# Kernel optimization log

Hardware: AMD Instinct MI355X
Metric: run time of the kernel (lower is better)

The kernel has to match this reference:

```python
import math
import jax, jax.numpy as jnp
import numpy as np


def _procrustes_R(H):
    # H: [B, 3, 3]. Rotation R = V @ U^T with reflection fix (det(R) >= 0),
    # matching torch.svd convention (v = V, not V^T).
    u, s, vh = jnp.linalg.svd(H)
    v = jnp.swapaxes(vh, -1, -2)                       # [B,3,3]
    r = jnp.einsum('bij,bkj->bik', v, u)               # V @ U^T
    det = jnp.linalg.det(r)                            # [B]
    sign = jnp.where(det < 0, -1.0, 1.0)               # flip last column of V (reflect = diag(1,1,-1))
    flip = jnp.stack([jnp.ones_like(sign), jnp.ones_like(sign), sign], axis=-1)[:, None, :]
    v = v * flip
    return jnp.einsum('bij,bkj->bik', v, u)


def setup_inputs() -> dict:
    key = jax.random.key(0)
    k1, k2, k3, k4 = jax.random.split(key, 4)
    B, D, N, M = 8, 512, 2048, 2048
    return {
        'src_embedding': jax.random.normal(k1, (B, D, N), dtype=jnp.float32),
        'tgt_embedding': jax.random.normal(k2, (B, D, M), dtype=jnp.float32),
        'src': jax.random.normal(k3, (B, 3, N), dtype=jnp.float32),
        'tgt': jax.random.normal(k4, (B, 3, M), dtype=jnp.float32),
    }


def reference(src_embedding, tgt_embedding, src, tgt):
    d_k = src_embedding.shape[1]
    # attention correspondence: scores[b,n,m]
    scores = jnp.einsum('bdn,bdm->bnm', src_embedding, tgt_embedding) / math.sqrt(d_k)
    scores = jax.nn.softmax(scores, axis=2)
    # soft correspondence of src points in tgt: [B,3,N]
    src_corr = jnp.einsum('bdm,bnm->bdn', tgt, scores)
    src_mean = src.mean(axis=2, keepdims=True)          # [B,3,1]
    src_centered = src - src_mean
    src_corr_centered = src_corr - src_corr.mean(axis=2, keepdims=True)
    H = jnp.einsum('bin,bjn->bij', src_centered, src_corr_centered)  # [B,3,3]
    R = _procrustes_R(H)
    t = jnp.einsum('bij,bjk->bik', -R, src_mean) + tgt.mean(axis=2, keepdims=True)
    return R, t.reshape(src.shape[0], 3)
```

## Files before the change

kernel.cpp:

```cpp
#include <hip/hip_runtime.h>
#include <hip/hip_bf16.h>

#define BQ 8
#define DIM 512
#define NN 2048
#define MM 2048
#define MSPLIT 16

typedef __attribute__((ext_vector_type(8))) short short8;
typedef __attribute__((ext_vector_type(8))) unsigned short ushort8;
typedef __attribute__((ext_vector_type(4))) float floatx4;

#define GLOAD_LDS(gp, lp) \
    __builtin_amdgcn_global_load_lds( \
        (const __attribute__((address_space(1))) void*)(gp), \
        (__attribute__((address_space(3))) void*)(lp), 16, 0, 0)


static __device__ __forceinline__ unsigned short f2bf(float x) {
    __hip_bfloat16 h = __float2bfloat16(x);
    return *(unsigned short*)&h;
}

__global__ __launch_bounds__(256) void transpose_cast_kernel(
    const float* __restrict__ src_emb,
    const float* __restrict__ tgt_emb,
    __hip_bfloat16* __restrict__ Abf,
    __hip_bfloat16* __restrict__ Bbf)
{
    const int n0 = blockIdx.x * 64;
    const int d0 = blockIdx.y * 64;
    const int b  = blockIdx.z & 7;
    const int which = blockIdx.z >> 3;

    const float* in = (which == 0 ? src_emb : tgt_emb) + (size_t)b * DIM * NN;
    __hip_bfloat16* out = (which == 0 ? Abf : Bbf) + (size_t)b * NN * DIM;

    __shared__ float tl[64][65];

    const int t = threadIdx.x;

    {
        const int u = t & 15;
        const int r = t >> 4;
        #pragma unroll
        for (int rr = r; rr < 64; rr += 16) {
            float4 v = *(const float4*)&in[(size_t)(d0 + rr) * NN + n0 + u * 4];
            tl[rr][u * 4 + 0] = v.x;
            tl[rr][u * 4 + 1] = v.y;
            tl[rr][u * 4 + 2] = v.z;
            tl[rr][u * 4 + 3] = v.w;
        }
    }
    __syncthreads();

    {
        const int u = t & 7;
        const int r = t >> 3;
        #pragma unroll
        for (int rn = r; rn < 64; rn += 32) {
            ushort8 o;
            #pragma unroll
            for (int j = 0; j < 8; j++)
                o[j] = f2bf(tl[u * 8 + j][rn]);
            *(ushort8*)&out[(size_t)(n0 + rn) * DIM + d0 + u * 8] = o;
        }
    }
}

__global__ __launch_bounds__(256, 2) void attn_mfma_kernel(
    const __hip_bfloat16* __restrict__ Abf,
    const __hip_bfloat16* __restrict__ Bbf,
    const float* __restrict__ tgt,
    float* __restrict__ part)
{
    const int nt = blockIdx.x;
    const int qt = blockIdx.y;
    const int b  = blockIdx.z;
    const int t  = threadIdx.x;
    const int wave = t >> 6;
    const int lane = t & 63;
    const int lm   = lane & 15;
    const int quad = lane >> 4;
    const int wn   = wave * 32;

    __shared__ short As[128 * 64];
    __shared__ short Bs[128 * 64];

    const __hip_bfloat16* Abase = Abf + ((size_t)(b * NN + nt * 128)) * DIM;
    const int m0 = qt * 128;
    const __hip_bfloat16* Bbase = Bbf + ((size_t)(b * MM + m0)) * DIM;
    const float* Tb = tgt + (size_t)b * 3 * MM;

    const float SCALE = 0.044194173824159216f * 1.4426950408889634f;

    const int r8 = lane >> 3;
    const int c8 = lane & 7;
    const int cc = c8 ^ r8;
    const __hip_bfloat16* gA = Abase + (size_t)(wn + r8) * DIM + cc * 8;
    const __hip_bfloat16* gB = Bbase + (size_t)(wn + r8) * DIM + cc * 8;
    short* lA = &As[wn * 64];
    short* lB = &Bs[wn * 64];

    floatx4 acc[2][8];
    #pragma unroll
    for (int i = 0; i < 2; i++)
        #pragma unroll
        for (int j = 0; j < 8; j++)
            acc[i][j] = (floatx4){0.f, 0.f, 0.f, 0.f};

    #pragma unroll
    for (int kt = 0; kt < 8; kt++) {
        #pragma unroll
        for (int i = 0; i < 4; i++) {
            GLOAD_LDS(gA + kt * 64 + (size_t)i * 8 * DIM, lA + i * 512);
            GLOAD_LDS(gB + kt * 64 + (size_t)i * 8 * DIM, lB + i * 512);
        }
        __syncthreads();

        #pragma unroll
        for (int ks = 0; ks < 2; ks++) {
            const int pc = (((ks * 4 + quad) ^ (lane & 7)) * 8);
            short8 af0 = *(const short8*)&As[(wn +      lm) * 64 + pc];
            short8 af1 = *(const short8*)&As[(wn + 16 + lm) * 64 + pc];
            #pragma unroll
            for (int j = 0; j < 8; j++) {
                short8 bf = *(const short8*)&Bs[(j * 16 + lm) * 64 + pc];
                acc[0][j] = __builtin_amdgcn_mfma_f32_16x16x32_bf16(af0, bf, acc[0][j], 0, 0, 0);
                acc[1][j] = __builtin_amdgcn_mfma_f32_16x16x32_bf16(af1, bf, acc[1][j], 0, 0, 0);
            }
        }
        __syncthreads();
    }

    float v0[8], v1[8], v2[8];
    #pragma unroll
    for (int j = 0; j < 8; j++) {
        int vc = m0 + j * 16 + lm;
        v0[j] = Tb[vc];
        v1[j] = Tb[MM + vc];
        v2[j] = Tb[2 * MM + vc];
    }

    const size_t slot = (size_t)(b * MSPLIT + qt) * NN;
    #pragma unroll
    for (int i = 0; i < 2; i++) {
        float l4[4] = {0,0,0,0};
        float o0[4] = {0,0,0,0};
        float o1[4] = {0,0,0,0};
        float o2[4] = {0,0,0,0};
        #pragma unroll
        for (int j = 0; j < 8; j++) {
            #pragma unroll
            for (int r = 0; r < 4; r++) {
                float e = __builtin_amdgcn_exp2f(acc[i][j][r] * SCALE);
                l4[r] += e;
                o0[r] += e * v0[j];
                o1[r] += e * v1[j];
                o2[r] += e * v2[j];
            }
        }
        #pragma unroll
        for (int m = 1; m <= 8; m <<= 1) {
            #pragma unroll
            for (int r = 0; r < 4; r++) {
                l4[r] += __shfl_xor(l4[r], m);
                o0[r] += __shfl_xor(o0[r], m);
                o1[r] += __shfl_xor(o1[r], m);
                o2[r] += __shfl_xor(o2[r], m);
            }
        }
        if (lm == 0) {
            #pragma unroll
            for (int r = 0; r < 4; r++) {
                int n = nt * 128 + wn + i * 16 + quad * 4 + r;
                ((float4*)part)[slot + n] = make_float4(l4[r], o0[r], o1[r], o2[r]);
            }
        }
    }
}

__global__ __launch_bounds__(256) void head_kernel(
    const float* __restrict__ ws,
    const float* __restrict__ src,
    const float* __restrict__ tgt,
    float* __restrict__ out)
{
    const int b = blockIdx.x;
    const int t = threadIdx.x;

    float pp[3][3] = {};
    float sc[3] = {0,0,0};
    float ss[3] = {0,0,0};
    float st[3] = {0,0,0};

    const float4* w4 = (const float4*)ws;
    const float* S = src + (size_t)b * 3 * NN;
    const float* T = tgt + (size_t)b * 3 * MM;

    for (int n = t; n < NN; n += 256) {
        float l = 0.f, y0 = 0.f, y1 = 0.f, y2 = 0.f;
        #pragma unroll
        for (int q = 0; q < 16; q++) {
            float4 p = w4[(size_t)(b * 16 + q) * NN + n];
            l += p.x; y0 += p.y; y1 += p.z; y2 += p.w;
        }
        float inv = 1.0f / l;
        float c0 = y0 * inv;
        float c1 = y1 * inv;
        float c2 = y2 * inv;
        float s0 = S[n], s1 = S[NN + n], s2 = S[2 * NN + n];
        sc[0] += c0; sc[1] += c1; sc[2] += c2;
        ss[0] += s0; ss[1] += s1; ss[2] += s2;
        st[0] += T[n]; st[1] += T[MM + n]; st[2] += T[2 * MM + n];
        pp[0][0] += s0 * c0; pp[0][1] += s0 * c1; pp[0][2] += s0 * c2;
        pp[1][0] += s1 * c0; pp[1][1] += s1 * c1; pp[1][2] += s1 * c2;
        pp[2][0] += s2 * c0; pp[2][1] += s2 * c1; pp[2][2] += s2 * c2;
    }

    float vals[18];
    vals[0] = ss[0]; vals[1] = ss[1]; vals[2] = ss[2];
    vals[3] = sc[0]; vals[4] = sc[1]; vals[5] = sc[2];
    vals[6] = st[0]; vals[7] = st[1]; vals[8] = st[2];
    vals[9]  = pp[0][0]; vals[10] = pp[0][1]; vals[11] = pp[0][2];
    vals[12] = pp[1][0]; vals[13] = pp[1][1]; vals[14] = pp[1][2];
    vals[15] = pp[2][0]; vals[16] = pp[2][1]; vals[17] = pp[2][2];

    #pragma unroll
    for (int m = 1; m <= 32; m <<= 1)
        #pragma unroll
        for (int c = 0; c < 18; c++)
            vals[c] += __shfl_xor(vals[c], m);

    __shared__ float warr[4][18];
    const int wave = t >> 6;
    if ((t & 63) == 0)
        #pragma unroll
        for (int c = 0; c < 18; c++) warr[wave][c] = vals[c];
    __syncthreads();

    if (t == 0) {
        float res[18];
        #pragma unroll
        for (int c = 0; c < 18; c++)
            res[c] = warr[0][c] + warr[1][c] + warr[2][c] + warr[3][c];

        const float invN = 1.0f / (float)NN;
        float mus[3], muc[3], mut[3], H[3][3];
        for (int i = 0; i < 3; i++) {
            mus[i] = res[i] * invN;
            muc[i] = res[3 + i] * invN;
            mut[i] = res[6 + i] * invN;
        }
        for (int i = 0; i < 3; i++)
            for (int j = 0; j < 3; j++)
                H[i][j] = res[9 + i * 3 + j] - (float)NN * mus[i] * muc[j];

        float A[3][3];
        for (int i = 0; i < 3; i++)
            for (int j = 0; j < 3; j++)
                A[i][j] = H[0][i] * H[0][j] + H[1][i] * H[1][j] + H[2][i] * H[2][j];

        float V[3][3] = {{1,0,0},{0,1,0},{0,0,1}};
        for (int sweep = 0; sweep < 6; sweep++) {
            for (int pi = 0; pi < 3; pi++) {
                int p = (pi < 2) ? 0 : 1;
                int q = (pi == 0) ? 1 : 2;
                float apq = A[p][q];
                if (fabsf(apq) < 1e-30f) continue;
                float tau = (A[q][q] - A[p][p]) / (2.0f * apq);
                float tt = (tau >= 0.0f) ? 1.0f / (tau + sqrtf(1.0f + tau * tau))
                                         : -1.0f / (-tau + sqrtf(1.0f + tau * tau));
                float c = 1.0f / sqrtf(1.0f + tt * tt);
                float s = tt * c;
                for (int k = 0; k < 3; k++) {
                    float akp = A[k][p], akq = A[k][q];
                    A[k][p] = c * akp - s * akq;
                    A[k][q] = s * akp + c * akq;
                }
                for (int k = 0; k < 3; k++) {
                    float apk = A[p][k], aqk = A[q][k];
                    A[p][k] = c * apk - s * aqk;
                    A[q][k] = s * apk + c * aqk;
                }
                for (int k = 0; k < 3; k++) {
                    float vkp = V[k][p], vkq = V[k][q];
                    V[k][p] = c * vkp - s * vkq;
                    V[k][q] = s * vkp + c * vkq;
                }
            }
        }

        float lam[3] = {A[0][0], A[1][1], A[2][2]};
        int idx[3] = {0, 1, 2};
        for (int a = 0; a < 2; a++)
            for (int bb = 0; bb < 2 - a; bb++)
                if (lam[idx[bb]] < lam[idx[bb + 1]]) { int tmp = idx[bb]; idx[bb] = idx[bb + 1]; idx[bb + 1] = tmp; }

        float Vc[3][3], U[3][3];
        for (int c = 0; c < 3; c++) {
            float sv = sqrtf(fmaxf(lam[idx[c]], 0.0f));
            float isv = 1.0f / fmaxf(sv, 1e-20f);
            for (int r = 0; r < 3; r++) {
                Vc[r][c] = V[r][idx[c]];
                U[r][c] = (H[r][0] * V[0][idx[c]] + H[r][1] * V[1][idx[c]] + H[r][2] * V[2][idx[c]]) * isv;
            }
        }

        {
            float nrm = rsqrtf(U[0][0]*U[0][0] + U[1][0]*U[1][0] + U[2][0]*U[2][0]);
            for (int r = 0; r < 3; r++) U[r][0] *= nrm;
            float d01 = U[0][0]*U[0][1] + U[1][0]*U[1][1] + U[2][0]*U[2][1];
            for (int r = 0; r < 3; r++) U[r][1] -= d01 * U[r][0];
            nrm = rsqrtf(U[0][1]*U[0][1] + U[1][1]*U[1][1] + U[2][1]*U[2][1]);
            for (int r = 0; r < 3; r++) U[r][1] *= nrm;
            float d02 = U[0][0]*U[0][2] + U[1][0]*U[1][2] + U[2][0]*U[2][2];
            float d12 = U[0][1]*U[0][2] + U[1][1]*U[1][2] + U[2][1]*U[2][2];
            for (int r = 0; r < 3; r++) U[r][2] -= d02 * U[r][0] + d12 * U[r][1];
            nrm = rsqrtf(U[0][2]*U[0][2] + U[1][2]*U[1][2] + U[2][2]*U[2][2]);
            for (int r = 0; r < 3; r++) U[r][2] *= nrm;
        }

        float det = H[0][0]*(H[1][1]*H[2][2] - H[1][2]*H[2][1])
                  - H[0][1]*(H[1][0]*H[2][2] - H[1][2]*H[2][0])
                  + H[0][2]*(H[1][0]*H[2][1] - H[1][1]*H[2][0]);
        float sgn = (det < 0.0f) ? -1.0f : 1.0f;

        float R[3][3];
        for (int i = 0; i < 3; i++)
            for (int j = 0; j < 3; j++)
                R[i][j] = Vc[i][0]*U[j][0] + Vc[i][1]*U[j][1] + sgn * Vc[i][2]*U[j][2];

        for (int i = 0; i < 3; i++)
            for (int j = 0; j < 3; j++)
                out[b * 9 + i * 3 + j] = R[i][j];
        for (int i = 0; i < 3; i++)
            out[BQ * 9 + b * 3 + i] = mut[i] - (R[i][0]*mus[0] + R[i][1]*mus[1] + R[i][2]*mus[2]);
    }
}

extern "C" void kernel_launch(void* const* d_in, const int* in_sizes, int n_in,
                              void* d_out, int out_size, void* d_ws, size_t ws_size,
                              hipStream_t stream) {
    const float* src_emb = (const float*)d_in[0];
    const float* tgt_emb = (const float*)d_in[1];
    const float* src     = (const float*)d_in[2];
    const float* tgt     = (const float*)d_in[3];
    float* out = (float*)d_out;

    float* part = (float*)d_ws;
    __hip_bfloat16* Abf = (__hip_bfloat16*)((char*)d_ws + (4 << 20));
    __hip_bfloat16* Bbf = (__hip_bfloat16*)((char*)d_ws + (20 << 20));

    dim3 gridT(NN / 64, DIM / 64, 2 * BQ);
    transpose_cast_kernel<<<gridT, 256, 0, stream>>>(src_emb, tgt_emb, Abf, Bbf);

    dim3 gridA(NN / 128, MSPLIT, BQ);
    attn_mfma_kernel<<<gridA, 256, 0, stream>>>(Abf, Bbf, tgt, part);

    head_kernel<<<BQ, 256, 0, stream>>>(part, src, tgt, out);
}
```

Baseline: 175.9 us.

## Use 2x2 wave tiling with A fragments loaded directly from global

Changes the per-block wave layout from four 32x128 strips to a 2x2 grid of 64x64 tiles, so each wave reuses each B fragment across four A rows and reads less from LDS per MFMA. A fragments are now loaded straight from global memory into registers instead of being staged through LDS, which halves the shared-memory footprint. The two M-halves' partial softmax sums are combined in LDS before one store. The costs are uncoalesced direct global A loads with exposed latency, plus an extra barrier and reduction step.

```diff
diff --git a/kernel.cpp b/kernel.cpp
--- a/kernel.cpp
+++ b/kernel.cpp
@@ -82,10 +82,11 @@
     const int lane = t & 63;
     const int lm   = lane & 15;
     const int quad = lane >> 4;
-    const int wn   = wave * 32;
-
-    __shared__ short As[128 * 64];
+    const int nh = (wave >> 1);
+    const int mh = (wave & 1);
+
     __shared__ short Bs[128 * 64];
+    __shared__ float4 sc4[2][128];
 
     const __hip_bfloat16* Abase = Abf + ((size_t)(b * NN + nt * 128)) * DIM;
     const int m0 = qt * 128;
@@ -96,61 +97,67 @@
 
     const int r8 = lane >> 3;
     const int c8 = lane & 7;
-    const int cc = c8 ^ r8;
-    const __hip_bfloat16* gA = Abase + (size_t)(wn + r8) * DIM + cc * 8;
-    const __hip_bfloat16* gB = Bbase + (size_t)(wn + r8) * DIM + cc * 8;
-    short* lA = &As[wn * 64];
-    short* lB = &Bs[wn * 64];
-
-    floatx4 acc[2][8];
-    #pragma unroll
-    for (int i = 0; i < 2; i++)
-        #pragma unroll
-        for (int j = 0; j < 8; j++)
+    const __hip_bfloat16* gB = Bbase + (size_t)(wave * 32 + r8) * DIM + (c8 ^ r8) * 8;
+    short* lB = &Bs[(wave * 32) * 64];
+
+    const __hip_bfloat16* gA[4];
+    #pragma unroll
+    for (int i = 0; i < 4; i++)
+        gA[i] = Abase + (size_t)(nh * 64 + i * 16 + lm) * DIM + quad * 8;
+
+    floatx4 acc[4][4];
+    #pragma unroll
+    for (int i = 0; i < 4; i++)
+        #pragma unroll
+        for (int j = 0; j < 4; j++)
             acc[i][j] = (floatx4){0.f, 0.f, 0.f, 0.f};
 
     #pragma unroll
     for (int kt = 0; kt < 8; kt++) {
         #pragma unroll
+        for (int i = 0; i < 4; i++)
+            GLOAD_LDS(gB + kt * 64 + (size_t)i * 8 * DIM, lB + i * 512);
+
+        short8 af0[4], af1[4];
+        #pragma unroll
         for (int i = 0; i < 4; i++) {
-            GLOAD_LDS(gA + kt * 64 + (size_t)i * 8 * DIM, lA + i * 512);
-            GLOAD_LDS(gB + kt * 64 + (size_t)i * 8 * DIM, lB + i * 512);
+            af0[i] = *(const short8*)(gA[i] + kt * 64);
+            af1[i] = *(const short8*)(gA[i] + kt * 64 + 32);
         }
         __syncthreads();
 
         #pragma unroll
         for (int ks = 0; ks < 2; ks++) {
-            const int pc = (((ks * 4 + quad) ^ (lane & 7)) * 8);
-            short8 af0 = *(const short8*)&As[(wn +      lm) * 64 + pc];
-            short8 af1 = *(const short8*)&As[(wn + 16 + lm) * 64 + pc];
-            #pragma unroll
-            for (int j = 0; j < 8; j++) {
-                short8 bf = *(const short8*)&Bs[(j * 16 + lm) * 64 + pc];
-                acc[0][j] = __builtin_amdgcn_mfma_f32_16x16x32_bf16(af0, bf, acc[0][j], 0, 0, 0);
-                acc[1][j] = __builtin_amdgcn_mfma_f32_16x16x32_bf16(af1, bf, acc[1][j], 0, 0, 0);
+            const int pc = (((ks * 4 + quad) ^ (lm & 7)) * 8);
+            #pragma unroll
+            for (int j = 0; j < 4; j++) {
+                short8 bf = *(const short8*)&Bs[(mh * 64 + j * 16 + lm) * 64 + pc];
+                #pragma unroll
+                for (int i = 0; i < 4; i++)
+                    acc[i][j] = __builtin_amdgcn_mfma_f32_16x16x32_bf16(
+                        ks ? af1[i] : af0[i], bf, acc[i][j], 0, 0, 0);
             }
         }
         __syncthreads();
     }
 
-    float v0[8], v1[8], v2[8];
-    #pragma unroll
-    for (int j = 0; j < 8; j++) {
-        int vc = m0 + j * 16 + lm;
+    float v0[4], v1[4], v2[4];
+    #pragma unroll
+    for (int j = 0; j < 4; j++) {
+        int vc = m0 + mh * 64 + j * 16 + lm;
         v0[j] = Tb[vc];
         v1[j] = Tb[MM + vc];
         v2[j] = Tb[2 * MM + vc];
     }
 
-    const size_t slot = (size_t)(b * MSPLIT + qt) * NN;
-    #pragma unroll
-    for (int i = 0; i < 2; i++) {
+    #pragma unroll
+    for (int i = 0; i < 4; i++) {
         float l4[4] = {0,0,0,0};
         float o0[4] = {0,0,0,0};
         float o1[4] = {0,0,0,0};
         float o2[4] = {0,0,0,0};
         #pragma unroll
-        for (int j = 0; j < 8; j++) {
+        for (int j = 0; j < 4; j++) {
             #pragma unroll
             for (int r = 0; r < 4; r++) {
                 float e = __builtin_amdgcn_exp2f(acc[i][j][r] * SCALE);
@@ -172,11 +179,17 @@
         }
         if (lm == 0) {
             #pragma unroll
-            for (int r = 0; r < 4; r++) {
-                int n = nt * 128 + wn + i * 16 + quad * 4 + r;
-                ((float4*)part)[slot + n] = make_float4(l4[r], o0[r], o1[r], o2[r]);
-            }
-        }
+            for (int r = 0; r < 4; r++)
+                sc4[mh][nh * 64 + i * 16 + quad * 4 + r] =
+                    make_float4(l4[r], o0[r], o1[r], o2[r]);
+        }
+    }
+    __syncthreads();
+
+    if (t < 128) {
+        float4 a = sc4[0][t], c = sc4[1][t];
+        ((float4*)part)[(size_t)(b * MSPLIT + qt) * NN + nt * 128 + t] =
+            make_float4(a.x + c.x, a.y + c.y, a.z + c.z, a.w + c.w);
     }
 }
 
```

Result: slower. 210.4 us (+19.6%).
